# Kernel optimization log

Hardware: AMD Instinct MI355X
Metric: run time of the kernel (lower is better)

Reference implementation:

```python
import jax, jax.numpy as jnp
import numpy as np

B, T, C, H = 4, 4096, 512, 64  # batch, seq(patches), n_embed, head_size

def setup_inputs() -> dict:
    key = jax.random.key(0)
    kx, kk, kq, kv = jax.random.split(key, 4)
    x = jax.random.normal(kx, (B, T, C), dtype=jnp.float32)
    # torch nn.Linear(n_embed, head_size).weight is [H, C]; store transposed [C, H]
    Wk = jax.random.normal(kk, (C, H), dtype=jnp.float32) / np.sqrt(C)
    Wq = jax.random.normal(kq, (C, H), dtype=jnp.float32) / np.sqrt(C)
    Wv = jax.random.normal(kv, (C, H), dtype=jnp.float32) / np.sqrt(C)
    return {"x": x, "Wk": Wk, "Wq": Wq, "Wv": Wv}

def reference(x, Wk, Wq, Wv):
    Bn, Tn, Cn = x.shape
    k = x @ Wk  # [B,T,H]
    q = x @ Wq
    v = x @ Wv
    # NOTE: original scales by C**-0.5 with C = n_embed (input dim), not head_size
    scores = jnp.einsum('bth,bsh->bts', q, k) * (Cn ** -0.5)  # [B,T,T]
    causal = jnp.tril(jnp.ones((Tn, Tn), dtype=bool))
    scores = jnp.where(causal, scores, -jnp.inf)
    attn = jax.nn.softmax(scores, axis=-1)
    return jnp.einsum('bts,bsh->bth', attn, v)  # [B,T,H]
```

## Files before the change

### kernel.cpp

```cpp
#include <hip/hip_runtime.h>
#include <hip/hip_bf16.h>

#define Tt 4096

typedef __bf16 bf16;
typedef __attribute__((ext_vector_type(8))) __bf16 bf16x8;
typedef __attribute__((ext_vector_type(4))) __bf16 bf16x4;
typedef __attribute__((ext_vector_type(4))) float f32x4;


__global__ __launch_bounds__(256) void wt_kernel(const float* __restrict__ Wk,
                                                 const float* __restrict__ Wq,
                                                 const float* __restrict__ Wv,
                                                 bf16* __restrict__ wt) {
  int idx = blockIdx.x * 256 + threadIdx.x;
  int mat = idx >> 15;
  int rem = idx & 32767;
  int n = rem >> 9;
  int k = rem & 511;
  const float* W = (mat == 0) ? Wk : (mat == 1) ? Wq : Wv;
  float v = W[k * 64 + n];
  if (mat == 1) v *= 0.044194173824159216f;
  wt[idx] = (bf16)v;
}

__global__ __launch_bounds__(256) void proj_kernel(const float* __restrict__ x,
                                                   const bf16* __restrict__ wt,
                                                   bf16* __restrict__ Kb,
                                                   bf16* __restrict__ Qb,
                                                   bf16* __restrict__ VTb) {
  __shared__ __attribute__((aligned(16))) bf16 xs[16][520];
  int tid = threadIdx.x;
  int row0 = blockIdx.x * 16;

  int sr = tid >> 4, sc = (tid & 15) * 4;
  const float* xr = x + (size_t)(row0 + sr) * 512;
#pragma unroll
  for (int j = 0; j < 8; ++j) {
    f32x4 a = *(const f32x4*)(xr + sc + j * 64);
    bf16x4 h;
#pragma unroll
    for (int e = 0; e < 4; ++e) h[e] = (bf16)a[e];
    *(bf16x4*)&xs[sr][sc + j * 64] = h;
  }
  __syncthreads();

  int wave = tid >> 6, lane = tid & 63, m = lane & 15, quad = lane >> 4;
  f32x4 acc[3];
#pragma unroll
  for (int i = 0; i < 3; ++i) acc[i] = (f32x4){0.f, 0.f, 0.f, 0.f};

#pragma unroll 4
  for (int kk = 0; kk < 512; kk += 32) {
    bf16x8 af = *(const bf16x8*)&xs[m][kk + quad * 8];
#pragma unroll
    for (int i = 0; i < 3; ++i) {
      int nt = wave * 3 + i;
      bf16x8 bfr = *(const bf16x8*)(wt + (nt >> 2) * 32768 +
                                    (((nt & 3) * 16) + m) * 512 + kk + quad * 8);
      acc[i] = __builtin_amdgcn_mfma_f32_16x16x32_bf16(af, bfr, acc[i], 0, 0, 0);
    }
  }

  int b = row0 >> 12, tloc = row0 & 4095;
#pragma unroll
  for (int i = 0; i < 3; ++i) {
    int nt = wave * 3 + i, mat = nt >> 2, n0 = (nt & 3) * 16;
    if (mat == 2) {
      bf16x4 pv;
#pragma unroll
      for (int r = 0; r < 4; ++r) pv[r] = (bf16)acc[i][r];
      *(bf16x4*)&VTb[((size_t)b * 64 + n0 + m) * 4096 + tloc + quad * 4] = pv;
    } else {
      bf16* dst = (mat == 0) ? Kb : Qb;
#pragma unroll
      for (int r = 0; r < 4; ++r)
        dst[(size_t)(row0 + quad * 4 + r) * 64 + n0 + m] = (bf16)acc[i][r];
    }
  }
}

__global__ __launch_bounds__(256, 4) void attn_kernel(const bf16* __restrict__ Qb,
                                                      const bf16* __restrict__ Kb,
                                                      const bf16* __restrict__ VTb,
                                                      bf16* __restrict__ Opart,
                                                      float* __restrict__ Lpart,
                                                      float* __restrict__ out) {
  __shared__ __attribute__((aligned(16))) bf16 Kt[2][64][72];
  __shared__ __attribute__((aligned(16))) bf16 Vt[2][64][72];

  int tid = threadIdx.x, wave = tid >> 6, lane = tid & 63;
  int m = lane & 15, quad = lane >> 4, kq = quad * 8;
  int r_ = tid >> 2, seg = tid & 3;

  int uu = 1151 - (int)blockIdx.x;
  int b = uu / 288, u2 = uu % 288;
  int g = 0;
  while (u2 >= 4 * (g + 1) * (g + 2)) ++g;
  int rr = u2 - 4 * g * (g + 1);
  int qi = 8 * g + rr / (g + 1);
  int c = rr % (g + 1);
  int t0 = qi * 64;
  int s_beg = c * 512;
  int niter = (min(s_beg + 512, t0 + 64) - s_beg) >> 6;

  const bf16* Qp = Qb + ((size_t)b * Tt + t0 + wave * 16 + m) * 64;
  bf16x8 aq0 = *(const bf16x8*)(Qp + kq);
  bf16x8 aq1 = *(const bf16x8*)(Qp + 32 + kq);

  bf16x8 onesb;
#pragma unroll
  for (int j = 0; j < 8; ++j) onesb[j] = (bf16)1.0f;

  f32x4 o[4];
#pragma unroll
  for (int i = 0; i < 4; ++i) o[i] = (f32x4){0.f, 0.f, 0.f, 0.f};
  f32x4 lsum = (f32x4){0.f, 0.f, 0.f, 0.f};

  const bf16* Kbase = Kb + (size_t)b * (Tt * 64);
  const bf16* VTbase = VTb + (size_t)b * (64 * Tt);

  {
    const bf16* ks = Kbase + (size_t)(s_beg + r_) * 64 + seg * 16;
    bf16x8 k0 = *(const bf16x8*)ks;
    bf16x8 k1 = *(const bf16x8*)(ks + 8);
    const bf16* vs = VTbase + (size_t)r_ * Tt + s_beg + seg * 16;
    bf16x8 v0 = *(const bf16x8*)vs;
    bf16x8 v1 = *(const bf16x8*)(vs + 8);
    *(bf16x8*)&Kt[0][r_][seg * 16] = k0;
    *(bf16x8*)&Kt[0][r_][seg * 16 + 8] = k1;
    *(bf16x8*)&Vt[0][r_][seg * 16] = v0;
    *(bf16x8*)&Vt[0][r_][seg * 16 + 8] = v1;
  }

  bf16x8 k0, k1, v0, v1;
  for (int i = 0; i < niter; ++i) {
    int s0 = s_beg + i * 64;
    int cur = i & 1, nxt = cur ^ 1;
    __syncthreads();

    if (i + 1 < niter) {
      int sn = s0 + 64;
      const bf16* ks2 = Kbase + (size_t)(sn + r_) * 64 + seg * 16;
      k0 = *(const bf16x8*)ks2;
      k1 = *(const bf16x8*)(ks2 + 8);
      const bf16* vs2 = VTbase + (size_t)r_ * Tt + sn + seg * 16;
      v0 = *(const bf16x8*)vs2;
      v1 = *(const bf16x8*)(vs2 + 8);
    }

    f32x4 s[4];
#pragma unroll
    for (int nt = 0; nt < 4; ++nt) {
      bf16x8 b0 = *(const bf16x8*)&Kt[cur][nt * 16 + m][kq];
      bf16x8 b1 = *(const bf16x8*)&Kt[cur][nt * 16 + m][32 + kq];
      f32x4 sa = (f32x4){0.f, 0.f, 0.f, 0.f};
      sa = __builtin_amdgcn_mfma_f32_16x16x32_bf16(aq0, b0, sa, 0, 0, 0);
      sa = __builtin_amdgcn_mfma_f32_16x16x32_bf16(aq1, b1, sa, 0, 0, 0);
      s[nt] = sa;
    }

    if (s0 + 64 > t0) {
#pragma unroll
      for (int nt = 0; nt < 4; ++nt) {
        int col = s0 + nt * 16 + m;
#pragma unroll
        for (int r = 0; r < 4; ++r) {
          int row = t0 + wave * 16 + quad * 4 + r;
          if (col > row) s[nt][r] = -1e30f;
        }
      }
    }

    bf16(*Pl)[72] = &Kt[nxt][wave * 16];
#pragma unroll
    for (int nt = 0; nt < 4; ++nt)
#pragma unroll
      for (int r = 0; r < 4; ++r)
        Pl[quad * 4 + r][nt * 16 + m] = (bf16)__expf(s[nt][r]);

#pragma unroll
    for (int ch = 0; ch < 2; ++ch) {
      bf16x8 ap = *(const bf16x8*)&Pl[m][ch * 32 + kq];
      lsum = __builtin_amdgcn_mfma_f32_16x16x32_bf16(ap, onesb, lsum, 0, 0, 0);
#pragma unroll
      for (int nt = 0; nt < 4; ++nt) {
        bf16x8 bv = *(const bf16x8*)&Vt[cur][nt * 16 + m][ch * 32 + kq];
        o[nt] = __builtin_amdgcn_mfma_f32_16x16x32_bf16(ap, bv, o[nt], 0, 0, 0);
      }
    }

    if (i + 1 < niter) {
      *(bf16x8*)&Kt[nxt][r_][seg * 16] = k0;
      *(bf16x8*)&Kt[nxt][r_][seg * 16 + 8] = k1;
      *(bf16x8*)&Vt[nxt][r_][seg * 16] = v0;
      *(bf16x8*)&Vt[nxt][r_][seg * 16 + 8] = v1;
    }
  }

  int rl0 = wave * 16 + quad * 4;
  if (g == 0) {
    float* op = out + ((size_t)b * Tt + t0) * 64;
#pragma unroll
    for (int r = 0; r < 4; ++r) {
      float inv = 1.0f / lsum[r];
#pragma unroll
      for (int nt = 0; nt < 4; ++nt)
        op[(size_t)(rl0 + r) * 64 + nt * 16 + m] = o[nt][r] * inv;
    }
  } else {
    int p = b * 288 + 4 * g * (g + 1) + (qi - 8 * g) * (g + 1) + c;
    bf16* Op = Opart + (size_t)p * 4096;
#pragma unroll
    for (int r = 0; r < 4; ++r)
#pragma unroll
      for (int nt = 0; nt < 4; ++nt)
        Op[(rl0 + r) * 64 + nt * 16 + m] = (bf16)o[nt][r];
    if (m == 0) {
#pragma unroll
      for (int r = 0; r < 4; ++r) Lpart[p * 64 + rl0 + r] = lsum[r];
    }
  }
}

__global__ __launch_bounds__(256) void combine_kernel(const bf16* __restrict__ Opart,
                                                      const float* __restrict__ Lpart,
                                                      float* __restrict__ out) {
  int blk = blockIdx.x;
  int b = blk / 224, rem = blk % 224;
  int qi = 8 + (rem >> 2), rq = rem & 3;
  int g = qi >> 3, nc = g + 1;
  int pb = b * 288 + 4 * g * (g + 1) + (qi - 8 * g) * (g + 1);
  int t = threadIdx.x, col = t & 63, rl = t >> 6;
#pragma unroll
  for (int rr = 0; rr < 4; ++rr) {
    int row64 = rq * 16 + rl * 4 + rr;
    float L = 0.f, acc = 0.f;
    for (int cc = 0; cc < nc; ++cc) {
      L += Lpart[(pb + cc) * 64 + row64];
      acc += (float)Opart[(size_t)(pb + cc) * 4096 + row64 * 64 + col];
    }
    out[((size_t)b * Tt + qi * 64 + row64) * 64 + col] = acc / L;
  }
}

extern "C" void kernel_launch(void* const* d_in, const int* in_sizes, int n_in,
                              void* d_out, int out_size, void* d_ws, size_t ws_size,
                              hipStream_t stream) {
  const float* x = (const float*)d_in[0];
  const float* Wk = (const float*)d_in[1];
  const float* Wq = (const float*)d_in[2];
  const float* Wv = (const float*)d_in[3];
  float* out = (float*)d_out;

  char* w = (char*)d_ws;
  bf16* wt = (bf16*)w;
  bf16* Kb = (bf16*)(w + 196608);
  bf16* Qb = (bf16*)(w + 2293760);
  bf16* VTb = (bf16*)(w + 4390912);
  bf16* Opart = (bf16*)(w + 6488064);
  float* Lpart = (float*)(w + 15925248);

  wt_kernel<<<384, 256, 0, stream>>>(Wk, Wq, Wv, wt);
  proj_kernel<<<1024, 256, 0, stream>>>(x, wt, Kb, Qb, VTb);
  attn_kernel<<<1152, 256, 0, stream>>>(Qb, Kb, VTb, Opart, Lpart, out);
  combine_kernel<<<896, 256, 0, stream>>>(Opart, Lpart, out);
}
```

Before: 138.5 us.

## Enlarge attention query tile to 128 rows with 256-key chunks per block

Each attention block now handles 128 query rows: every wave owns two 16-row fragments, so each K/V tile loaded into shared memory feeds twice as much MFMA work. Key splits shrink to 256-column chunks, and the work decomposition, partial-output layout and combine kernel are reworked to match. K and V loading is split by wave so half the waves load K and half load V. This cuts global and LDS traffic per flop, at the cost of more registers (launch bounds drop to 3 blocks per CU) and different load balance across blocks.

Measured after the change: 163.1 us. +17.8%, slower.

```diff
diff --git a/kernel.cpp b/kernel.cpp
--- a/kernel.cpp
+++ b/kernel.cpp
@@ -80,7 +80,7 @@
   }
 }
 
-__global__ __launch_bounds__(256, 4) void attn_kernel(const bf16* __restrict__ Qb,
+__global__ __launch_bounds__(256, 3) void attn_kernel(const bf16* __restrict__ Qb,
                                                       const bf16* __restrict__ Kb,
                                                       const bf16* __restrict__ VTb,
                                                       bf16* __restrict__ Opart,
@@ -91,49 +91,60 @@
 
   int tid = threadIdx.x, wave = tid >> 6, lane = tid & 63;
   int m = lane & 15, quad = lane >> 4, kq = quad * 8;
-  int r_ = tid >> 2, seg = tid & 3;
-
-  int uu = 1151 - (int)blockIdx.x;
-  int b = uu / 288, u2 = uu % 288;
-  int g = 0;
-  while (u2 >= 4 * (g + 1) * (g + 2)) ++g;
-  int rr = u2 - 4 * g * (g + 1);
-  int qi = 8 * g + rr / (g + 1);
-  int c = rr % (g + 1);
-  int t0 = qi * 64;
-  int s_beg = c * 512;
-  int niter = (min(s_beg + 512, t0 + 64) - s_beg) >> 6;
-
-  const bf16* Qp = Qb + ((size_t)b * Tt + t0 + wave * 16 + m) * 64;
-  bf16x8 aq0 = *(const bf16x8*)(Qp + kq);
-  bf16x8 aq1 = *(const bf16x8*)(Qp + 32 + kq);
+
+  int uu = 1087 - (int)blockIdx.x;
+  int b = uu & 3;
+  int u2 = uu >> 2;
+  int qi = 0;
+  for (;;) {
+    int sz = (qi >> 1) + 1;
+    if (u2 < sz) break;
+    u2 -= sz;
+    ++qi;
+  }
+  int c = u2;
+  int g = qi >> 1;
+  int t0 = qi * 128;
+  int s_beg = c * 256;
+  int niter = (min(s_beg + 256, t0 + 128) - s_beg) >> 6;
+
+  const bf16* Qp = Qb + ((size_t)b * Tt + t0 + wave * 32) * 64;
+  bf16x8 aq[2][2];
+#pragma unroll
+  for (int rf = 0; rf < 2; ++rf)
+#pragma unroll
+    for (int ch = 0; ch < 2; ++ch)
+      aq[rf][ch] = *(const bf16x8*)(Qp + (size_t)(rf * 16 + m) * 64 + ch * 32 + kq);
 
   bf16x8 onesb;
 #pragma unroll
   for (int j = 0; j < 8; ++j) onesb[j] = (bf16)1.0f;
 
-  f32x4 o[4];
-#pragma unroll
-  for (int i = 0; i < 4; ++i) o[i] = (f32x4){0.f, 0.f, 0.f, 0.f};
-  f32x4 lsum = (f32x4){0.f, 0.f, 0.f, 0.f};
-
-  const bf16* Kbase = Kb + (size_t)b * (Tt * 64);
-  const bf16* VTbase = VTb + (size_t)b * (64 * Tt);
+  f32x4 o[2][4];
+#pragma unroll
+  for (int rf = 0; rf < 2; ++rf)
+#pragma unroll
+    for (int dt = 0; dt < 4; ++dt) o[rf][dt] = (f32x4){0.f, 0.f, 0.f, 0.f};
+  f32x4 ls[2];
+  ls[0] = ls[1] = (f32x4){0.f, 0.f, 0.f, 0.f};
+
+  const bf16* Kbase = Kb + (size_t)b * Tt * 64;
+  const bf16* VTbase = VTb + (size_t)b * 64 * Tt;
+
+  int sr = lane >> 1, sh = (lane & 1) * 32;
+  bool isK = wave < 2;
+  int rowoff = (wave & 1) * 32;
 
   {
-    const bf16* ks = Kbase + (size_t)(s_beg + r_) * 64 + seg * 16;
-    bf16x8 k0 = *(const bf16x8*)ks;
-    bf16x8 k1 = *(const bf16x8*)(ks + 8);
-    const bf16* vs = VTbase + (size_t)r_ * Tt + s_beg + seg * 16;
-    bf16x8 v0 = *(const bf16x8*)vs;
-    bf16x8 v1 = *(const bf16x8*)(vs + 8);
-    *(bf16x8*)&Kt[0][r_][seg * 16] = k0;
-    *(bf16x8*)&Kt[0][r_][seg * 16 + 8] = k1;
-    *(bf16x8*)&Vt[0][r_][seg * 16] = v0;
-    *(bf16x8*)&Vt[0][r_][seg * 16 + 8] = v1;
-  }
-
-  bf16x8 k0, k1, v0, v1;
+    const bf16* src = isK ? (Kbase + (size_t)(s_beg + rowoff + sr) * 64 + sh)
+                          : (VTbase + (size_t)(rowoff + sr) * Tt + s_beg + sh);
+    bf16* dst = isK ? &Kt[0][rowoff + sr][sh] : &Vt[0][rowoff + sr][sh];
+#pragma unroll
+    for (int j = 0; j < 4; ++j)
+      *(bf16x8*)(dst + j * 8) = *(const bf16x8*)(src + j * 8);
+  }
+
+  bf16x8 pf[4];
   for (int i = 0; i < niter; ++i) {
     int s0 = s_beg + i * 64;
     int cur = i & 1, nxt = cur ^ 1;
@@ -141,84 +152,109 @@
 
     if (i + 1 < niter) {
       int sn = s0 + 64;
-      const bf16* ks2 = Kbase + (size_t)(sn + r_) * 64 + seg * 16;
-      k0 = *(const bf16x8*)ks2;
-      k1 = *(const bf16x8*)(ks2 + 8);
-      const bf16* vs2 = VTbase + (size_t)r_ * Tt + sn + seg * 16;
-      v0 = *(const bf16x8*)vs2;
-      v1 = *(const bf16x8*)(vs2 + 8);
-    }
-
-    f32x4 s[4];
+      const bf16* src = isK ? (Kbase + (size_t)(sn + rowoff + sr) * 64 + sh)
+                            : (VTbase + (size_t)(rowoff + sr) * Tt + sn + sh);
+#pragma unroll
+      for (int j = 0; j < 4; ++j) pf[j] = *(const bf16x8*)(src + j * 8);
+    }
+
+    f32x4 s[2][4];
 #pragma unroll
     for (int nt = 0; nt < 4; ++nt) {
       bf16x8 b0 = *(const bf16x8*)&Kt[cur][nt * 16 + m][kq];
       bf16x8 b1 = *(const bf16x8*)&Kt[cur][nt * 16 + m][32 + kq];
-      f32x4 sa = (f32x4){0.f, 0.f, 0.f, 0.f};
-      sa = __builtin_amdgcn_mfma_f32_16x16x32_bf16(aq0, b0, sa, 0, 0, 0);
-      sa = __builtin_amdgcn_mfma_f32_16x16x32_bf16(aq1, b1, sa, 0, 0, 0);
-      s[nt] = sa;
+#pragma unroll
+      for (int rf = 0; rf < 2; ++rf) {
+        f32x4 sa = (f32x4){0.f, 0.f, 0.f, 0.f};
+        sa = __builtin_amdgcn_mfma_f32_16x16x32_bf16(aq[rf][0], b0, sa, 0, 0, 0);
+        sa = __builtin_amdgcn_mfma_f32_16x16x32_bf16(aq[rf][1], b1, sa, 0, 0, 0);
+        s[rf][nt] = sa;
+      }
     }
 
     if (s0 + 64 > t0) {
 #pragma unroll
-      for (int nt = 0; nt < 4; ++nt) {
-        int col = s0 + nt * 16 + m;
-#pragma unroll
-        for (int r = 0; r < 4; ++r) {
-          int row = t0 + wave * 16 + quad * 4 + r;
-          if (col > row) s[nt][r] = -1e30f;
+      for (int rf = 0; rf < 2; ++rf)
+#pragma unroll
+        for (int nt = 0; nt < 4; ++nt) {
+          int col = s0 + nt * 16 + m;
+#pragma unroll
+          for (int r = 0; r < 4; ++r) {
+            int row = t0 + wave * 32 + rf * 16 + quad * 4 + r;
+            if (col > row) s[rf][nt][r] = -1e30f;
+          }
         }
+    }
+
+    bf16(*Pl)[72] = isK ? &Kt[nxt][rowoff] : &Vt[nxt][rowoff];
+#pragma unroll
+    for (int rf = 0; rf < 2; ++rf)
+#pragma unroll
+      for (int nt = 0; nt < 4; ++nt)
+#pragma unroll
+        for (int r = 0; r < 4; ++r)
+          Pl[rf * 16 + quad * 4 + r][nt * 16 + m] = (bf16)__expf(s[rf][nt][r]);
+
+    bf16x8 ap[2][2];
+#pragma unroll
+    for (int rf = 0; rf < 2; ++rf)
+#pragma unroll
+      for (int ch = 0; ch < 2; ++ch)
+        ap[rf][ch] = *(const bf16x8*)&Pl[rf * 16 + m][ch * 32 + kq];
+#pragma unroll
+    for (int rf = 0; rf < 2; ++rf)
+#pragma unroll
+      for (int ch = 0; ch < 2; ++ch)
+        ls[rf] = __builtin_amdgcn_mfma_f32_16x16x32_bf16(ap[rf][ch], onesb, ls[rf], 0, 0, 0);
+#pragma unroll
+    for (int dt = 0; dt < 4; ++dt) {
+      bf16x8 v0 = *(const bf16x8*)&Vt[cur][dt * 16 + m][kq];
+      bf16x8 v1 = *(const bf16x8*)&Vt[cur][dt * 16 + m][32 + kq];
+#pragma unroll
+      for (int rf = 0; rf < 2; ++rf) {
+        o[rf][dt] = __builtin_amdgcn_mfma_f32_16x16x32_bf16(ap[rf][0], v0, o[rf][dt], 0, 0, 0);
+        o[rf][dt] = __builtin_amdgcn_mfma_f32_16x16x32_bf16(ap[rf][1], v1, o[rf][dt], 0, 0, 0);
       }
     }
 
-    bf16(*Pl)[72] = &Kt[nxt][wave * 16];
-#pragma unroll
-    for (int nt = 0; nt < 4; ++nt)
-#pragma unroll
-      for (int r = 0; r < 4; ++r)
-        Pl[quad * 4 + r][nt * 16 + m] = (bf16)__expf(s[nt][r]);
-
-#pragma unroll
-    for (int ch = 0; ch < 2; ++ch) {
-      bf16x8 ap = *(const bf16x8*)&Pl[m][ch * 32 + kq];
-      lsum = __builtin_amdgcn_mfma_f32_16x16x32_bf16(ap, onesb, lsum, 0, 0, 0);
-#pragma unroll
-      for (int nt = 0; nt < 4; ++nt) {
-        bf16x8 bv = *(const bf16x8*)&Vt[cur][nt * 16 + m][ch * 32 + kq];
-        o[nt] = __builtin_amdgcn_mfma_f32_16x16x32_bf16(ap, bv, o[nt], 0, 0, 0);
+    if (i + 1 < niter) {
+      bf16* dst = isK ? &Kt[nxt][rowoff + sr][sh] : &Vt[nxt][rowoff + sr][sh];
+#pragma unroll
+      for (int j = 0; j < 4; ++j) *(bf16x8*)(dst + j * 8) = pf[j];
+    }
+  }
+
+  if (g == 0) {
+    float* op = out + ((size_t)b * Tt + t0 + wave * 32) * 64;
+#pragma unroll
+    for (int rf = 0; rf < 2; ++rf)
+#pragma unroll
+      for (int r = 0; r < 4; ++r) {
+        float inv = 1.0f / ls[rf][r];
+        int row = rf * 16 + quad * 4 + r;
+#pragma unroll
+        for (int dt = 0; dt < 4; ++dt)
+          op[(size_t)row * 64 + dt * 16 + m] = o[rf][dt][r] * inv;
       }
-    }
-
-    if (i + 1 < niter) {
-      *(bf16x8*)&Kt[nxt][r_][seg * 16] = k0;
-      *(bf16x8*)&Kt[nxt][r_][seg * 16 + 8] = k1;
-      *(bf16x8*)&Vt[nxt][r_][seg * 16] = v0;
-      *(bf16x8*)&Vt[nxt][r_][seg * 16 + 8] = v1;
-    }
-  }
-
-  int rl0 = wave * 16 + quad * 4;
-  if (g == 0) {
-    float* op = out + ((size_t)b * Tt + t0) * 64;
-#pragma unroll
-    for (int r = 0; r < 4; ++r) {
-      float inv = 1.0f / lsum[r];
-#pragma unroll
-      for (int nt = 0; nt < 4; ++nt)
-        op[(size_t)(rl0 + r) * 64 + nt * 16 + m] = o[nt][r] * inv;
-    }
   } else {
-    int p = b * 288 + 4 * g * (g + 1) + (qi - 8 * g) * (g + 1) + c;
-    bf16* Op = Opart + (size_t)p * 4096;
-#pragma unroll
-    for (int r = 0; r < 4; ++r)
-#pragma unroll
-      for (int nt = 0; nt < 4; ++nt)
-        Op[(rl0 + r) * 64 + nt * 16 + m] = (bf16)o[nt][r];
+    int pbase = (qi & 1) ? (g + 1) * (g + 1) : g * (g + 1);
+    int p = b * 272 + pbase + c;
+    bf16* Op = Opart + (size_t)p * 8192;
+#pragma unroll
+    for (int rf = 0; rf < 2; ++rf)
+#pragma unroll
+      for (int r = 0; r < 4; ++r) {
+        int row = wave * 32 + rf * 16 + quad * 4 + r;
+#pragma unroll
+        for (int dt = 0; dt < 4; ++dt)
+          Op[row * 64 + dt * 16 + m] = (bf16)o[rf][dt][r];
+      }
     if (m == 0) {
 #pragma unroll
-      for (int r = 0; r < 4; ++r) Lpart[p * 64 + rl0 + r] = lsum[r];
+      for (int rf = 0; rf < 2; ++rf)
+#pragma unroll
+        for (int r = 0; r < 4; ++r)
+          Lpart[p * 128 + wave * 32 + rf * 16 + quad * 4 + r] = ls[rf][r];
     }
   }
 }
@@ -227,20 +263,21 @@
                                                       const float* __restrict__ Lpart,
                                                       float* __restrict__ out) {
   int blk = blockIdx.x;
-  int b = blk / 224, rem = blk % 224;
-  int qi = 8 + (rem >> 2), rq = rem & 3;
-  int g = qi >> 3, nc = g + 1;
-  int pb = b * 288 + 4 * g * (g + 1) + (qi - 8 * g) * (g + 1);
-  int t = threadIdx.x, col = t & 63, rl = t >> 6;
-#pragma unroll
-  for (int rr = 0; rr < 4; ++rr) {
-    int row64 = rq * 16 + rl * 4 + rr;
+  int b = blk / 120, rem = blk % 120;
+  int qi = 2 + (rem >> 2), rq = rem & 3;
+  int g = qi >> 1, nc = g + 1;
+  int pbase = (qi & 1) ? (g + 1) * (g + 1) : g * (g + 1);
+  int pb = b * 272 + pbase;
+  int col = threadIdx.x & 63, rl = threadIdx.x >> 6;
+#pragma unroll
+  for (int pass = 0; pass < 8; ++pass) {
+    int row = rq * 32 + pass * 4 + rl;
     float L = 0.f, acc = 0.f;
     for (int cc = 0; cc < nc; ++cc) {
-      L += Lpart[(pb + cc) * 64 + row64];
-      acc += (float)Opart[(size_t)(pb + cc) * 4096 + row64 * 64 + col];
-    }
-    out[((size_t)b * Tt + qi * 64 + row64) * 64 + col] = acc / L;
+      L += Lpart[(pb + cc) * 128 + row];
+      acc += (float)Opart[(size_t)(pb + cc) * 8192 + row * 64 + col];
+    }
+    out[((size_t)b * Tt + qi * 128 + row) * 64 + col] = acc / L;
   }
 }
 
@@ -259,10 +296,10 @@
   bf16* Qb = (bf16*)(w + 2293760);
   bf16* VTb = (bf16*)(w + 4390912);
   bf16* Opart = (bf16*)(w + 6488064);
-  float* Lpart = (float*)(w + 15925248);
+  float* Lpart = (float*)(w + 24313856);
 
   wt_kernel<<<384, 256, 0, stream>>>(Wk, Wq, Wv, wt);
   proj_kernel<<<1024, 256, 0, stream>>>(x, wt, Kb, Qb, VTb);
-  attn_kernel<<<1152, 256, 0, stream>>>(Qb, Kb, VTb, Opart, Lpart, out);
-  combine_kernel<<<896, 256, 0, stream>>>(Opart, Lpart, out);
-}
+  attn_kernel<<<1088, 256, 0, stream>>>(Qb, Kb, VTb, Opart, Lpart, out);
+  combine_kernel<<<480, 256, 0, stream>>>(Opart, Lpart, out);
+}
```
